# Kernel tuning notes

Hardware: AMD Instinct MI355X
Metric: run time of the kernel (lower is better)

The kernel has to match this reference:

```python
import jax, jax.numpy as jnp
import numpy as np

EPS = 1e-5
ALPHA = 0.05   # propalpha
GDEP = 2       # gcn_depth
LAYERS = 3     # gcn_layers
NUM_TCN = 2    # num_layer tcn units per encoder


def conv1x1(W, b, x):
    # 1x1 Conv2d on [B,C,N,1]: pure channel mix
    return jnp.einsum('oc,bcnl->bonl', W, x) + b[None, :, None, None]


def tcn_unit(Wf, bf, Wg, bg, h):
    # gated TCN unit: tanh(filter) * sigmoid(gate), 1x1 convs (L==1)
    return jnp.tanh(conv1x1(Wf, bf, h)) * jax.nn.sigmoid(conv1x1(Wg, bg, h))


def mixprop(x, A, W, b):
    # MTGNN mixprop: add self-loops, row-normalize, gdep propagation steps,
    # concat hops on channel dim, 1x1 conv mlp. A: [N,N] or [B,N,N].
    N = A.shape[-1]
    A = A + jnp.eye(N, dtype=A.dtype)
    A = A / A.sum(-1, keepdims=True)
    h = x
    outs = [h]
    for _ in range(GDEP):
        if A.ndim == 2:
            hn = jnp.einsum('vw,bcwl->bcvl', A, h)
        else:
            hn = jnp.einsum('bvw,bcwl->bcvl', A, h)
        h = ALPHA * x + (1.0 - ALPHA) * hn
        outs.append(h)
    ho = jnp.concatenate(outs, axis=1)  # [B,(GDEP+1)*C,N,1]
    return conv1x1(W, b, ho)


def layernorm(x, w, b):
    # LayerNorm over (C,N,1) of [B,C,N,1]; idx=arange(N) selects full affine
    mu = x.mean(axis=(1, 2, 3), keepdims=True)
    var = x.var(axis=(1, 2, 3), keepdims=True)
    return (x - mu) / jnp.sqrt(var + EPS) * w[None] + b[None]


def setup_inputs() -> dict:
    key = jax.random.key(0)
    B, N, E, H, S, T = 8, 2048, 32, 128, 256, 12
    ks = jax.random.split(key, 32)
    s = 0.05
    inp = {
        'x': jax.random.normal(ks[0], (B, E, N, 1), jnp.float32),
        'dy_graph': jax.random.uniform(ks[1], (B, N, N), jnp.float32),
        'static_graph': jax.random.uniform(ks[2], (N, N), jnp.float32),
        'spatial_emb': jax.random.normal(ks[3], (B, 32, N, 1), jnp.float32),
        'temporal_d_emb': jax.random.normal(ks[4], (B, 32, N, 1), jnp.float32),
        'temporal_w_emb': jax.random.normal(ks[5], (B, 32, N, 1), jnp.float32),
        'enc_Wf': s * jax.random.normal(ks[6], (LAYERS, NUM_TCN, H, H), jnp.float32),
        'enc_bf': s * jax.random.normal(ks[7], (LAYERS, NUM_TCN, H), jnp.float32),
        'enc_Wg': s * jax.random.normal(ks[8], (LAYERS, NUM_TCN, H, H), jnp.float32),
        'enc_bg': s * jax.random.normal(ks[9], (LAYERS, NUM_TCN, H), jnp.float32),
        'skip_W': s * jax.random.normal(ks[10], (LAYERS, S, H), jnp.float32),
        'skip_b': s * jax.random.normal(ks[11], (LAYERS, S), jnp.float32),
        'norm_w': jnp.ones((LAYERS, E, N, 1), jnp.float32),
        'norm_b': jnp.zeros((LAYERS, E, N, 1), jnp.float32),
        'g0_W': s * jax.random.normal(ks[12], (LAYERS, E, (GDEP + 1) * E), jnp.float32),
        'g0_b': s * jax.random.normal(ks[13], (LAYERS, E), jnp.float32),
        'g1_W': s * jax.random.normal(ks[14], (LAYERS, E, (GDEP + 1) * E), jnp.float32),
        'g1_b': s * jax.random.normal(ks[15], (LAYERS, E), jnp.float32),
        'g2_W': s * jax.random.normal(ks[16], (LAYERS, E, (GDEP + 1) * E), jnp.float32),
        'g2_b': s * jax.random.normal(ks[17], (LAYERS, E), jnp.float32),
        'skipE_W': s * jax.random.normal(ks[18], (S, E), jnp.float32),
        'skipE_b': s * jax.random.normal(ks[19], (S,), jnp.float32),
        'end_W': s * jax.random.normal(ks[20], (T, S), jnp.float32),
        'end_b': s * jax.random.normal(ks[21], (T,), jnp.float32),
    }
    return inp


def reference(x, dy_graph, static_graph, spatial_emb, temporal_d_emb, temporal_w_emb,
              enc_Wf, enc_bf, enc_Wg, enc_bg, skip_W, skip_b, norm_w, norm_b,
              g0_W, g0_b, g1_W, g1_b, g2_W, g2_b, skipE_W, skipE_b, end_W, end_b):
    adp = dy_graph
    skip = 0.0
    for i in range(LAYERS):
        residual = x
        hidden = jnp.concatenate([x, spatial_emb, temporal_d_emb, temporal_w_emb], axis=1)
        for j in range(NUM_TCN):
            hidden = tcn_unit(enc_Wf[i, j], enc_bf[i, j], enc_Wg[i, j], enc_bg[i, j], hidden)
        skip = conv1x1(skip_W[i], skip_b[i], hidden) + skip
        x = (mixprop(x, static_graph, g0_W[i], g0_b[i])
             + mixprop(x, adp, g1_W[i], g1_b[i])
             + mixprop(x, jnp.swapaxes(adp, -1, -2), g2_W[i], g2_b[i]))
        x = x + residual
        x = jax.nn.relu(layernorm(x, norm_w[i], norm_b[i]))
    skip = conv1x1(skipE_W, skipE_b, x) + skip
    return conv1x1(end_W, end_b, skip)  # [B, seq_length, N, 1]
```

## Files before the change

### kernel.cpp

```cpp
#include <hip/hip_runtime.h>
#include <stdint.h>


typedef uint16_t u16;
typedef uint32_t u32;
typedef __attribute__((ext_vector_type(8))) short s8v;
typedef __attribute__((ext_vector_type(4))) float f4v;

#define MFMA16(a,b,c) __builtin_amdgcn_mfma_f32_16x16x32_bf16(a,b,c,0,0,0)

__device__ __forceinline__ float b2f(u16 u){ union{u32 i; float f;} x; x.i=(u32)u<<16; return x.f; }
__device__ __forceinline__ u16 f2b(float f){
  u32 u = __builtin_bit_cast(u32, f);
  u32 r = (u + 0x7fffu + ((u >> 16) & 1u)) >> 16;
  return (u16)r;
}

__global__ __launch_bounds__(256) void kdetect(const u16* __restrict__ x, int* __restrict__ flag)
{
  const int i = threadIdx.x;
  const uint4* p = (const uint4*)x;
  int cnt = 0;
  #pragma unroll
  for (int q = 0; q < 32; q++) {
    const uint4 v = p[i + q*256];
    const u32 w[4] = {v.x, v.y, v.z, v.w};
    #pragma unroll
    for (int e = 0; e < 4; e++) {
      if ((w[e] & 0x7F80u) == 0x7F80u) cnt++;
      if (((w[e] >> 16) & 0x7F80u) == 0x7F80u) cnt++;
    }
  }
  __shared__ int s[256];
  s[i] = cnt; __syncthreads();
  for (int st = 128; st; st >>= 1) { if (i < st) s[i] += s[i+st]; __syncthreads(); }
  if (i == 0) flag[0] = (s[0] > 0) ? 1 : 0;
}

__global__ __launch_bounds__(256) void kcvt4(const void* __restrict__ src, u16* __restrict__ dst,
                                             int n4, const int* __restrict__ flag)
{
  if (!*flag) return;
  const int i = blockIdx.x*256 + threadIdx.x;
  if (i >= n4) return;
  const float4 v = ((const float4*)src)[i];
  u16 o[4]; o[0]=f2b(v.x); o[1]=f2b(v.y); o[2]=f2b(v.z); o[3]=f2b(v.w);
  *(uint2*)(dst + (long)i*4) = *(uint2*)o;
}

struct CvtTab { const void* s[18]; u16* d[18]; int n4[18]; };
__global__ __launch_bounds__(256) void kcvt_small(CvtTab tb, const int* __restrict__ flag)
{
  const int e = blockIdx.y;
  const int i = blockIdx.x*256 + threadIdx.x;
  if (i >= tb.n4[e]) return;
  if (*flag) {
    const float4 v = ((const float4*)tb.s[e])[i];
    u16 o[4]; o[0]=f2b(v.x); o[1]=f2b(v.y); o[2]=f2b(v.z); o[3]=f2b(v.w);
    *(uint2*)(tb.d[e] + (long)i*4) = *(uint2*)o;
  } else {
    *(uint2*)(tb.d[e] + (long)i*4) = ((const uint2*)tb.s[e])[i];
  }
}

__global__ __launch_bounds__(256) void kcvtT(
    const void* __restrict__ src, u16* __restrict__ dyb, u16* __restrict__ dytb,
    float* __restrict__ rsum, float* __restrict__ csum, const int* __restrict__ flag)
{
  __shared__ alignas(16) u16 tt[64][112];
  const int tid = threadIdx.x;
  const int b = blockIdx.z;
  const long r0 = (long)blockIdx.y*64;
  const long c0 = (long)blockIdx.x*64;
  const int r = tid>>2, cg = (tid&3)*16;
  const long base = (long)b*4194304;
  const int fl = *flag;

  u16 v16[16];
  const long goff = base + (r0+r)*2048 + c0 + cg;
  if (fl) {
    const float* sp = (const float*)src + goff;
    #pragma unroll
    for (int q = 0; q < 4; q++) {
      const float4 f = ((const float4*)sp)[q];
      v16[q*4+0]=f2b(f.x); v16[q*4+1]=f2b(f.y); v16[q*4+2]=f2b(f.z); v16[q*4+3]=f2b(f.w);
    }
    *(uint4*)(dyb + goff)     = *(uint4*)&v16[0];
    *(uint4*)(dyb + goff + 8) = *(uint4*)&v16[8];
  } else {
    const u16* sp = (const u16*)src + goff;
    *(uint4*)&v16[0] = ((const uint4*)sp)[0];
    *(uint4*)&v16[8] = ((const uint4*)sp)[1];
  }
  float rs = 0.f;
  #pragma unroll
  for (int e = 0; e < 16; e++) {
    rs += b2f(v16[e]);
    const int c = cg + e;
    tt[c][r + ((c>>4)&3)*16] = v16[e];
  }
  rs += __shfl_down(rs, 2, 64);
  rs += __shfl_down(rs, 1, 64);
  if ((tid&3)==0) atomicAdd(rsum + b*2048 + r0 + r, rs);
  __syncthreads();

  const int c = tid>>2, rg = (tid&3)*16;
  const int sh = ((c>>4)&3)*16;
  u16 col[16];
  *(uint4*)&col[0] = *(const uint4*)&tt[c][sh + rg];
  *(uint4*)&col[8] = *(const uint4*)&tt[c][sh + rg + 8];
  float cs = 0.f;
  #pragma unroll
  for (int e = 0; e < 16; e++) cs += b2f(col[e]);
  cs += __shfl_down(cs, 2, 64);
  cs += __shfl_down(cs, 1, 64);
  u16* dp = dytb + base + (c0 + c)*2048 + r0 + rg;
  *(uint4*)(dp)     = *(uint4*)&col[0];
  *(uint4*)(dp + 8) = *(uint4*)&col[8];
  if ((tid&3)==0) atomicAdd(csum + b*2048 + c0 + c, cs);
}

__global__ void kfin(float* __restrict__ v){
  const int i = blockIdx.x*256 + threadIdx.x;
  v[i] = 1.f/(1.f + v[i]);
}

struct P3 {
  const u16* A0; const u16* A1; const u16* A2;
  const u16* A0alt; const u16* A1alt;
  const int* flag;
  long ab0, ab1, ab2;
  const u16* X0; const u16* X1; const u16* X2;
  const float* R0; const float* R1; const float* R2;
  long rb0, rb1, rb2;
  u16* O0; u16* O1; u16* O2;
};

template<int SHAREX>
__global__ __launch_bounds__(256) void kprop3(P3 p, long x_bs, long o_bs)
{
  constexpr int NS = SHAREX ? 5 : 9;
  __shared__ f4v red[4][6][64];
  const int tid = threadIdx.x, wave = tid>>6, lane = tid&63;
  const int lw = lane&15, quad = lane>>4;
  const int v0 = blockIdx.x*16;
  const int b = blockIdx.y;
  const long ko = (long)(wave*512 + quad*8);
  const int fl = *p.flag;
  const u16* A0g = fl ? p.A0 : p.A0alt;
  const u16* A1g = fl ? p.A1 : p.A1alt;
  const u16* ptr[9];
  ptr[0] = A0g + (long)b*p.ab0 + (long)(v0+lw)*2048 + ko;
  ptr[1] = A1g + (long)b*p.ab1 + (long)(v0+lw)*2048 + ko;
  ptr[2] = p.A2 + (long)b*p.ab2 + (long)(v0+lw)*2048 + ko;
  ptr[3] = p.X0 + (long)b*x_bs + (long)lw*2048 + ko;
  ptr[4] = p.X0 + (long)b*x_bs + (long)(16+lw)*2048 + ko;
  if (!SHAREX) {
    ptr[5] = p.X1 + (long)b*x_bs + (long)lw*2048 + ko;
    ptr[6] = p.X1 + (long)b*x_bs + (long)(16+lw)*2048 + ko;
    ptr[7] = p.X2 + (long)b*x_bs + (long)lw*2048 + ko;
    ptr[8] = p.X2 + (long)b*x_bs + (long)(16+lw)*2048 + ko;
  }
  f4v acc[6];
  #pragma unroll
  for (int t = 0; t < 6; t++) acc[t] = (f4v){0.f,0.f,0.f,0.f};
  s8v B0[NS][2], B1[NS][2];

  auto LD = [&](s8v (&B)[NS][2], int off){
    #pragma unroll
    for (int s = 0; s < NS; s++) {
      B[s][0] = *(const s8v*)(ptr[s] + off);
      B[s][1] = *(const s8v*)(ptr[s] + off + 32);
    }
  };
  auto FM = [&](s8v (&B)[NS][2]){
    #pragma unroll
    for (int u = 0; u < 2; u++) {
      if (SHAREX) {
        acc[0] = MFMA16(B[0][u], B[3][u], acc[0]);
        acc[1] = MFMA16(B[0][u], B[4][u], acc[1]);
        acc[2] = MFMA16(B[1][u], B[3][u], acc[2]);
        acc[3] = MFMA16(B[1][u], B[4][u], acc[3]);
        acc[4] = MFMA16(B[2][u], B[3][u], acc[4]);
        acc[5] = MFMA16(B[2][u], B[4][u], acc[5]);
      } else {
        acc[0] = MFMA16(B[0][u], B[3][u], acc[0]);
        acc[1] = MFMA16(B[0][u], B[4][u], acc[1]);
        acc[2] = MFMA16(B[1][u], B[5][u], acc[2]);
        acc[3] = MFMA16(B[1][u], B[6][u], acc[3]);
        acc[4] = MFMA16(B[2][u], B[7][u], acc[4]);
        acc[5] = MFMA16(B[2][u], B[8][u], acc[5]);
      }
    }
  };

  LD(B0, 0);
  #pragma unroll 1
  for (int i = 0; i < 3; i++) {
    LD(B1, 64);
    FM(B0);
    LD(B0, 128);
    FM(B1);
    #pragma unroll
    for (int s = 0; s < NS; s++) ptr[s] += 128;
  }
  LD(B1, 64);
  FM(B0);
  FM(B1);

  #pragma unroll
  for (int t = 0; t < 6; t++) red[wave][t][lane] = acc[t];
  __syncthreads();
  if (wave < 3) {
    const int vb = v0 + quad*4;
    const u16* Xg   = (wave==0) ? p.X0 : (wave==1) ? (SHAREX ? p.X0 : p.X1) : (SHAREX ? p.X0 : p.X2);
    const float* Rg = (wave==0) ? p.R0 : (wave==1) ? p.R1 : p.R2;
    const long rbs  = (wave==0) ? p.rb0 : (wave==1) ? p.rb1 : p.rb2;
    u16* Og         = (wave==0) ? p.O0 : (wave==1) ? p.O1 : p.O2;
    #pragma unroll
    for (int nt = 0; nt < 2; nt++) {
      const int t = wave*2 + nt;
      f4v s = red[0][t][lane] + red[1][t][lane] + red[2][t][lane] + red[3][t][lane];
      const int c = nt*16 + lw;
      const u16* dp = Xg + (long)b*x_bs + (long)c*2048 + vb;
      const float* rp = Rg + (long)b*rbs + vb;
      u16 pk[4];
      #pragma unroll
      for (int r = 0; r < 4; r++) pk[r] = f2b((s[r] + b2f(dp[r])) * rp[r]);
      *(uint2*)(Og + (long)b*o_bs + (long)c*2048 + vb) = *(uint2*)pk;
    }
  }
}

template<int TRANSA, int MODE>
__global__ __launch_bounds__(256) void kprop(
    const u16* __restrict__ A, long a_bs, int lda, int K,
    const u16* __restrict__ X, long x_bs, int ldx,
    const u16* __restrict__ D, long d_bs,
    const float* __restrict__ rinv, long r_bs,
    const float* __restrict__ bias,
    u16* __restrict__ out0, float* __restrict__ out1, long o_bs)
{
  __shared__ u16 As[4][2][16][40];
  __shared__ f4v red[4][2][64];
  const int tid = threadIdx.x;
  const int wave = tid >> 6, lane = tid & 63;
  const int lw = lane & 15, quad = lane >> 4;
  const int v0 = blockIdx.x * 16;
  const int ball = blockIdx.z + blockIdx.y;
  const u16* Ab = A + (long)ball * a_bs;
  const u16* Xb = X + (long)ball * x_bs;
  const int KC = K >> 5;

  f4v acc0 = {0.f,0.f,0.f,0.f}, acc1 = {0.f,0.f,0.f,0.f};

  int r0, c0_;
  if (TRANSA == 0) { r0 = lane >> 2; c0_ = (lane & 3) * 8; }
  else             { r0 = lane >> 1; c0_ = (lane & 1) * 8; }

  int ci = wave;
  bool has = ci < KC;
  uint4 d = make_uint4(0,0,0,0);
  if (has) {
    d = (TRANSA == 0)
      ? *(const uint4*)(Ab + (long)(v0 + r0) * lda + ci * 32 + c0_)
      : *(const uint4*)(Ab + (long)(ci * 32 + r0) * lda + v0 + c0_);
  }
  int buf = 0;
  while (has) {
    if (TRANSA == 0) {
      *(uint4*)&As[wave][buf][r0][c0_] = d;
    } else {
      u16 tmp[8]; *(uint4*)tmp = d;
      #pragma unroll
      for (int e = 0; e < 8; e++) As[wave][buf][c0_ + e][r0] = tmp[e];
    }
    const int cn = ci + 4;
    const bool hn = cn < KC;
    if (hn) {
      d = (TRANSA == 0)
        ? *(const uint4*)(Ab + (long)(v0 + r0) * lda + cn * 32 + c0_)
        : *(const uint4*)(Ab + (long)(cn * 32 + r0) * lda + v0 + c0_);
    }
    s8v af = *(const s8v*)&As[wave][buf][lw][quad * 8];
    const u16* xk = Xb + ci * 32 + quad * 8;
    s8v b0 = *(const s8v*)(xk + (long)lw * ldx);
    s8v b1 = *(const s8v*)(xk + (long)(16 + lw) * ldx);
    acc0 = MFMA16(af, b0, acc0);
    acc1 = MFMA16(af, b1, acc1);
    ci = cn; has = hn; buf ^= 1;
  }
  red[wave][0][lane] = acc0;
  red[wave][1][lane] = acc1;
  __syncthreads();
  if (wave == 0) {
    const int vb = v0 + quad * 4;
    #pragma unroll
    for (int nt = 0; nt < 2; nt++) {
      f4v a = red[0][nt][lane] + red[1][nt][lane] + red[2][nt][lane] + red[3][nt][lane];
      const int c = nt * 16 + lw;
      const u16* dp = D + (long)ball * d_bs + (long)c * 2048 + vb;
      if (MODE == 0) {
        const float* rp = rinv + (long)ball * r_bs + vb;
        u16 pk[4];
        #pragma unroll
        for (int r = 0; r < 4; r++) pk[r] = f2b((a[r] + b2f(dp[r])) * rp[r]);
        *(uint2*)(out0 + (long)ball * o_bs + (long)c * 2048 + vb) = *(uint2*)pk;
      } else {
        const float bs = bias[c];
        float4 st;
        st.x = a[0] + bs + b2f(dp[0]);
        st.y = a[1] + bs + b2f(dp[1]);
        st.z = a[2] + bs + b2f(dp[2]);
        st.w = a[3] + bs + b2f(dp[3]);
        *(float4*)(out1 + (long)ball * o_bs + (long)c * 2048 + vb) = st;
      }
    }
  }
}

__global__ __launch_bounds__(256) void ktcn(
    const u16* __restrict__ H, const u16* __restrict__ Wf, const u16* __restrict__ bfv,
    const u16* __restrict__ Wg, const u16* __restrict__ bgv, u16* __restrict__ out)
{
  const int tid = threadIdx.x, wave = tid>>6, lane = tid&63, lw = lane&15, quad = lane>>4;
  const long j0 = (long)blockIdx.x*64 + wave*16;
  const f4v zero = {0.f,0.f,0.f,0.f};
  f4v accf[8], accg[8];
  #pragma unroll
  for (int nt=0; nt<8; nt++){ accf[nt] = zero; accg[nt] = zero; }
  const u16* Arow = H + (j0 + lw)*128 + quad*8;
  #pragma unroll
  for (int k0 = 0; k0 < 128; k0 += 32) {
    s8v a = *(const s8v*)(Arow + k0);
    #pragma unroll
    for (int nt = 0; nt < 8; nt++) {
      const int o = nt*16 + lw;
      s8v bf_ = *(const s8v*)(Wf + o*128 + k0 + quad*8);
      s8v bg_ = *(const s8v*)(Wg + o*128 + k0 + quad*8);
      accf[nt] = MFMA16(a, bf_, accf[nt]);
      accg[nt] = MFMA16(a, bg_, accg[nt]);
    }
  }
  #pragma unroll
  for (int nt = 0; nt < 8; nt++) {
    const int o = nt*16 + lw;
    const float fb = b2f(bfv[o]), gb = b2f(bgv[o]);
    #pragma unroll
    for (int rr = 0; rr < 4; rr++) {
      const long j = j0 + quad*4 + rr;
      const float f = accf[nt][rr] + fb, g = accg[nt][rr] + gb;
      const float e2 = __expf(2.f*f);
      const float th = 1.f - 2.f/(e2 + 1.f);
      const float sg = 1.f/(1.f + __expf(-g));
      out[j*128 + o] = f2b(th*sg);
    }
  }
}

__global__ __launch_bounds__(256) void kskip(
    const u16* __restrict__ A, int lda, int K,
    const u16* __restrict__ W, int ldb,
    const u16* __restrict__ bias,
    float* __restrict__ skipbuf, int addprev, int mode, u16* __restrict__ outb)
{
  const int tid = threadIdx.x, wave = tid>>6, lane = tid&63, lw = lane&15, quad = lane>>4;
  const long j0 = (long)blockIdx.x*64 + wave*16;
  const f4v zero = {0.f,0.f,0.f,0.f};
  f4v acc[16];
  #pragma unroll
  for (int nt=0; nt<16; nt++) acc[nt] = zero;
  const u16* Arow = A + (j0 + lw)*(long)lda + quad*8;
  for (int k0 = 0; k0 < K; k0 += 32) {
    s8v a = *(const s8v*)(Arow + k0);
    #pragma unroll
    for (int nt = 0; nt < 16; nt++) {
      const int o = nt*16 + lw;
      s8v b = *(const s8v*)(W + (long)o*ldb + k0 + quad*8);
      acc[nt] = MFMA16(a, b, acc[nt]);
    }
  }
  #pragma unroll
  for (int nt = 0; nt < 16; nt++) {
    const int o = nt*16 + lw;
    const float bv = b2f(bias[o]);
    #pragma unroll
    for (int rr = 0; rr < 4; rr++) {
      const long j = j0 + quad*4 + rr;
      float v = acc[nt][rr] + bv;
      if (addprev) v += skipbuf[j*256 + o];
      if (mode == 0) skipbuf[j*256 + o] = v;
      else           outb[j*256 + o] = f2b(v);
    }
  }
}

__global__ __launch_bounds__(256) void kend(
    const u16* __restrict__ A, const u16* __restrict__ W, const u16* __restrict__ bias,
    void* __restrict__ outv, const int* __restrict__ flag)
{
  const int tid = threadIdx.x, wave = tid>>6, lane = tid&63, lw = lane&15, quad = lane>>4;
  const long j0 = (long)blockIdx.x*64 + wave*16;
  f4v acc = {0.f,0.f,0.f,0.f};
  const u16* Arow = A + (j0 + lw)*256 + quad*8;
  #pragma unroll
  for (int k0 = 0; k0 < 256; k0 += 32) {
    s8v a = *(const s8v*)(Arow + k0);
    s8v b = {0,0,0,0,0,0,0,0};
    if (lw < 12) b = *(const s8v*)(W + lw*256 + k0 + quad*8);
    acc = MFMA16(a, b, acc);
  }
  if (lw < 12) {
    const float bv = b2f(bias[lw]);
    const int fl = *flag;
    #pragma unroll
    for (int rr = 0; rr < 4; rr++) {
      const long j = j0 + quad*4 + rr;
      const long oi = (j >> 11)*24576 + lw*2048 + (j & 2047);
      const float val = acc[rr] + bv;
      if (fl) ((float*)outv)[oi] = val;
      else    ((u16*)outv)[oi]   = f2b(val);
    }
  }
}

__global__ __launch_bounds__(256) void khid0(
    const void* __restrict__ x, const void* __restrict__ spat,
    const void* __restrict__ tde, const void* __restrict__ twe,
    u16* __restrict__ hid, u16* __restrict__ slot0, const int* __restrict__ flag)
{
  __shared__ u16 t[32][72];
  const int tid = threadIdx.x, b = blockIdx.y, v0 = blockIdx.x*64;
  const int fl = *flag;
  const void* srcs[4] = {x, spat, tde, twe};
  #pragma unroll
  for (int e = 0; e < 4; e++) {
    const int c = tid>>3, v8 = (tid&7)*8;
    const long boff = (long)c*2048 + v0 + v8;
    u16 o8[8];
    if (fl) {
      const float* sp = (const float*)srcs[e] + (long)b*65536 + boff;
      const float4 a = ((const float4*)sp)[0], bb = ((const float4*)sp)[1];
      o8[0]=f2b(a.x); o8[1]=f2b(a.y); o8[2]=f2b(a.z); o8[3]=f2b(a.w);
      o8[4]=f2b(bb.x); o8[5]=f2b(bb.y); o8[6]=f2b(bb.z); o8[7]=f2b(bb.w);
    } else {
      *(uint4*)o8 = *(const uint4*)((const u16*)srcs[e] + (long)b*65536 + boff);
    }
    if (e == 0) *(uint4*)(slot0 + (long)b*458752 + boff) = *(uint4*)o8;
    *(uint4*)&t[c][v8] = *(uint4*)o8;
    __syncthreads();
    const int jl = tid>>2, c8 = (tid&3)*8;
    u16 q8[8];
    #pragma unroll
    for (int i = 0; i < 8; i++) q8[i] = t[c8 + i][jl];
    *(uint4*)(hid + ((long)b*2048 + v0 + jl)*128 + e*32 + c8) = *(uint4*)q8;
    __syncthreads();
  }
}

__global__ __launch_bounds__(256) void krowsum(const u16* __restrict__ srcA, const u16* __restrict__ srcB,
                                               const int* __restrict__ flag,
                                               float* __restrict__ outv, int nrows)
{
  const u16* src = (*flag) ? srcA : srcB;
  const int wave = threadIdx.x>>6, lane = threadIdx.x&63;
  const int row = blockIdx.x*4 + wave;
  if (row >= nrows) return;
  const u16* p = src + (long)row*2048 + lane*8;
  float s = 0.f;
  #pragma unroll
  for (int it = 0; it < 4; it++) {
    u16 v[8]; *(uint4*)v = *(const uint4*)(p + it*512);
    #pragma unroll
    for (int e = 0; e < 8; e++) s += b2f(v[e]);
  }
  #pragma unroll
  for (int off = 32; off; off >>= 1) s += __shfl_down(s, off, 64);
  if (lane == 0) outv[row] = 1.f/(1.f + s);
}

__global__ __launch_bounds__(256) void kweff(
    const u16* __restrict__ g0W, const u16* __restrict__ g1W, const u16* __restrict__ g2W,
    const u16* __restrict__ g0b, const u16* __restrict__ g1b, const u16* __restrict__ g2b,
    int ioff, int boff, u16* __restrict__ weff, float* __restrict__ bw)
{
  const int idx = blockIdx.x*256 + threadIdx.x;
  if (idx < 32) bw[idx] = b2f(g0b[boff+idx]) + b2f(g1b[boff+idx]) + b2f(g2b[boff+idx]);
  if (idx >= 7168) return;
  const int o = idx / 224, m = idx % 224;
  const u16* Ws[3] = {g0W + ioff, g1W + ioff, g2W + ioff};
  float val;
  if (m < 32) {
    val = 0.f;
    #pragma unroll
    for (int g = 0; g < 3; g++) {
      const float w0 = b2f(Ws[g][o*96 + m]);
      const float w1 = b2f(Ws[g][o*96 + 32 + m]);
      const float w2 = b2f(Ws[g][o*96 + 64 + m]);
      val += w0 + 0.05f*(w1 + w2);
    }
  } else {
    const int f = (m - 32) >> 5, cc = m & 31;
    const int g = f >> 1, typ = f & 1;
    const float w1 = b2f(Ws[g][o*96 + 32 + cc]);
    const float w2 = b2f(Ws[g][o*96 + 64 + cc]);
    val = (typ == 0) ? (0.95f*w1 + 0.0475f*w2) : (0.9025f*w2);
  }
  weff[o*224 + m] = f2b(val);
}

__global__ __launch_bounds__(256) void kstats(const float* __restrict__ xpre, float* __restrict__ raw)
{
  const int b = blockIdx.y, tid = threadIdx.x;
  const float4* p = (const float4*)(xpre + (long)b*65536 + (long)blockIdx.x*8192);
  float s = 0.f, q = 0.f;
  #pragma unroll
  for (int i = 0; i < 8; i++) {
    const float4 v = p[tid + i*256];
    s += v.x + v.y + v.z + v.w;
    q += v.x*v.x + v.y*v.y + v.z*v.z + v.w*v.w;
  }
  __shared__ float ss[256], qq[256];
  ss[tid] = s; qq[tid] = q;
  __syncthreads();
  for (int st = 128; st; st >>= 1) {
    if (tid < st) { ss[tid] += ss[tid+st]; qq[tid] += qq[tid+st]; }
    __syncthreads();
  }
  if (tid == 0) { atomicAdd(raw + b*2, ss[0]); atomicAdd(raw + b*2 + 1, qq[0]); }
}

__global__ __launch_bounds__(256) void kapply(
    const float* __restrict__ xpre, const float* __restrict__ raw,
    const u16* __restrict__ nw, const u16* __restrict__ nb,
    u16* __restrict__ slot0, u16* __restrict__ hid)
{
  __shared__ u16 t[32][72];
  const int tid = threadIdx.x, b = blockIdx.y, v0 = blockIdx.x*64;
  const float mu = raw[b*2] * (1.f/65536.f);
  const float var = raw[b*2+1] * (1.f/65536.f) - mu*mu;
  const float rs = rsqrtf(var + 1e-5f);
  const int c = tid>>3, v8 = (tid&7)*8;
  const long boff = (long)c*2048 + v0 + v8;
  float4 xa = *(const float4*)(xpre + (long)b*65536 + boff);
  float4 xbv = *(const float4*)(xpre + (long)b*65536 + boff + 4);
  u16 wv[8], bv[8], o8[8];
  *(uint4*)wv = *(const uint4*)(nw + boff);
  *(uint4*)bv = *(const uint4*)(nb + boff);
  const float xs[8] = {xa.x, xa.y, xa.z, xa.w, xbv.x, xbv.y, xbv.z, xbv.w};
  #pragma unroll
  for (int e = 0; e < 8; e++) {
    float y = (xs[e] - mu) * rs * b2f(wv[e]) + b2f(bv[e]);
    y = fmaxf(y, 0.f);
    o8[e] = f2b(y);
    t[c][v8 + e] = o8[e];
  }
  *(uint4*)(slot0 + (long)b*458752 + boff) = *(uint4*)o8;
  __syncthreads();
  const int jl = tid>>2, c8 = (tid&3)*8;
  u16 q8[8];
  #pragma unroll
  for (int e = 0; e < 8; e++) q8[e] = t[c8 + e][jl];
  *(uint4*)(hid + ((long)b*2048 + v0 + jl)*128 + c8) = *(uint4*)q8;
}

extern "C" void kernel_launch(void* const* d_in, const int* in_sizes, int n_in,
                              void* d_out, int out_size, void* d_ws, size_t ws_size,
                              hipStream_t stream)
{
  (void)in_sizes; (void)n_in; (void)out_size; (void)ws_size;

  char* ws = (char*)d_ws;
  u16*   pbuf = (u16*)(ws + 0);
  u16*   hid  = (u16*)(ws + 7340032);
  u16*   hb1  = (u16*)(ws + 11534336);
  u16*   hb2  = (u16*)(ws + 15728640);
  float* skip = (float*)(ws + 19922944);
  u16*   xsb  = (u16*)(ws + 36700160);
  float* xpre = (float*)(ws + 45088768);
  u16*   weff = (u16*)(ws + 47185920);
  float* bw   = (float*)(ws + 47202304);
  float* rst  = (float*)(ws + 47203328);
  float* rdy  = (float*)(ws + 47211520);
  float* cdy  = (float*)(ws + 47277056);
  int*   flag = (int*)(ws + 47343616);
  float* raw  = (float*)(ws + 47343744);

  size_t coff = 50331648;
  auto alloc = [&](size_t elems) -> u16* {
    u16* p = (u16*)(ws + coff);
    coff += ((elems*2 + 255)/256)*256;
    return p;
  };
  u16* dyb   = alloc(33554432);
  u16* stgb  = alloc(4194304);
  u16* encWf = alloc(98304);
  u16* encbf = alloc(768);
  u16* encWg = alloc(98304);
  u16* encbg = alloc(768);
  u16* skW   = alloc(98304);
  u16* skb   = alloc(768);
  u16* nw    = alloc(196608);
  u16* nb    = alloc(196608);
  u16* g0W   = alloc(9216);
  u16* g0b   = alloc(96);
  u16* g1W   = alloc(9216);
  u16* g1b   = alloc(96);
  u16* g2W   = alloc(9216);
  u16* g2b   = alloc(96);
  u16* sEW   = alloc(8192);
  u16* sEb   = alloc(256);
  u16* eW    = alloc(3072);
  u16* eb    = alloc(12);
  u16* dytb  = alloc(33554432);

  hipLaunchKernelGGL(kdetect, dim3(1), dim3(256), 0, stream, (const u16*)d_in[0], flag);

  CvtTab tb;
  {
    const void* ss[18] = { d_in[6], d_in[7], d_in[8], d_in[9], d_in[10], d_in[11],
      d_in[12], d_in[13], d_in[14], d_in[15], d_in[16], d_in[17], d_in[18], d_in[19],
      d_in[20], d_in[21], d_in[22], d_in[23] };
    u16* dd[18] = { encWf, encbf, encWg, encbg, skW, skb, nw, nb,
      g0W, g0b, g1W, g1b, g2W, g2b, sEW, sEb, eW, eb };
    const int nn[18] = { 24576, 192, 24576, 192, 24576, 192, 49152, 49152,
      2304, 24, 2304, 24, 2304, 24, 2048, 64, 768, 3 };
    for (int e = 0; e < 18; e++) { tb.s[e] = ss[e]; tb.d[e] = dd[e]; tb.n4[e] = nn[e]; }
  }
  hipLaunchKernelGGL(kcvt_small, dim3(192, 18), dim3(256), 0, stream, tb, flag);
  hipLaunchKernelGGL(kcvt4, dim3(4096), dim3(256), 0, stream, d_in[2], stgb, 1048576, flag);

  hipMemsetAsync(rdy, 0, 131072, stream);
  hipMemsetAsync(raw, 0, 192, stream);
  hipLaunchKernelGGL(kcvtT, dim3(32,32,8), dim3(256), 0, stream,
      d_in[1], dyb, dytb, rdy, cdy, flag);
  hipLaunchKernelGGL(kfin, dim3(128), dim3(256), 0, stream, rdy);
  hipLaunchKernelGGL(krowsum, dim3(512), dim3(256), 0, stream,
      stgb, (const u16*)d_in[2], flag, rst, 2048);
  hipLaunchKernelGGL(khid0, dim3(32,8), dim3(256), 0, stream,
      d_in[0], d_in[3], d_in[4], d_in[5], hid, pbuf, flag);

  const long PB = 458752;
  const long SL = 65536;
  const long DYB = 4194304;

  for (int i = 0; i < 3; i++) {
    hipLaunchKernelGGL(ktcn, dim3(256), dim3(256), 0, stream,
        hid, encWf + (i*2+0)*16384, encbf + (i*2+0)*128, encWg + (i*2+0)*16384, encbg + (i*2+0)*128, hb1);
    hipLaunchKernelGGL(ktcn, dim3(256), dim3(256), 0, stream,
        hb1, encWf + (i*2+1)*16384, encbf + (i*2+1)*128, encWg + (i*2+1)*16384, encbg + (i*2+1)*128, hb2);
    hipLaunchKernelGGL(kskip, dim3(256), dim3(256), 0, stream,
        hb2, 128, 128, skW + i*32768, 128, skb + i*256, skip, (i>0)?1:0, 0, (u16*)nullptr);
    hipLaunchKernelGGL(kweff, dim3(28), dim3(256), 0, stream,
        g0W, g1W, g2W, g0b, g1b, g2b, i*3072, i*32, weff, bw);

    P3 p1;
    p1.A0 = stgb; p1.A1 = dyb; p1.A2 = dytb;
    p1.A0alt = (const u16*)d_in[2]; p1.A1alt = (const u16*)d_in[1]; p1.flag = flag;
    p1.ab0 = 0;   p1.ab1 = DYB; p1.ab2 = DYB;
    p1.X0 = pbuf; p1.X1 = pbuf; p1.X2 = pbuf;
    p1.R0 = rst;  p1.R1 = rdy;  p1.R2 = cdy;
    p1.rb0 = 0;   p1.rb1 = 2048; p1.rb2 = 2048;
    p1.O0 = pbuf + 1*SL; p1.O1 = pbuf + 3*SL; p1.O2 = pbuf + 5*SL;
    hipLaunchKernelGGL((kprop3<1>), dim3(128,8), dim3(256), 0, stream, p1, PB, PB);

    P3 p2 = p1;
    p2.X0 = pbuf + 1*SL; p2.X1 = pbuf + 3*SL; p2.X2 = pbuf + 5*SL;
    p2.O0 = pbuf + 2*SL; p2.O1 = pbuf + 4*SL; p2.O2 = pbuf + 6*SL;
    hipLaunchKernelGGL((kprop3<0>), dim3(128,8), dim3(256), 0, stream, p2, PB, PB);

    hipLaunchKernelGGL((kprop<1,1>), dim3(128,1,8), dim3(256), 0, stream,
        pbuf, PB, 2048, 224, weff, 0L, 224, pbuf, PB, (const float*)nullptr, 0L, bw, (u16*)nullptr, xpre, 65536L);
    hipLaunchKernelGGL(kstats, dim3(8,8), dim3(256), 0, stream, xpre, raw + i*16);
    hipLaunchKernelGGL(kapply, dim3(32,8), dim3(256), 0, stream,
        xpre, raw + i*16, nw + i*65536, nb + i*65536, pbuf, hid);
  }
  hipLaunchKernelGGL(kskip, dim3(256), dim3(256), 0, stream,
      hid, 128, 32, sEW, 32, sEb, skip, 1, 1, xsb);
  hipLaunchKernelGGL(kend, dim3(256), dim3(256), 0, stream, xsb, eW, eb, d_out, flag);
}
```

Baseline: 891.2 us.

## Split graph propagation per graph across grid z and reshape transpose and detect kernels

The three-graph propagation kernel is split so each block handles one graph (grid z = 3), cutting per-block register and load pressure and tripling the block count. In the first hop the shared X tile is now loaded separately for each graph, adding redundant X reads. The transpose kernel packs two rows per 32-bit LDS word with an XOR swizzle to avoid bank conflicts, and the NaN/Inf detection becomes a multi-block ballot plus atomicOr after a memset of the flag. The memset now covers 320 bytes from flag, which is assumed to also clear the raw stats buffer that previously had its own memset.

```diff
diff --git a/kernel.cpp b/kernel.cpp
--- a/kernel.cpp
+++ b/kernel.cpp
@@ -18,23 +18,17 @@
 
 __global__ __launch_bounds__(256) void kdetect(const u16* __restrict__ x, int* __restrict__ flag)
 {
-  const int i = threadIdx.x;
-  const uint4* p = (const uint4*)x;
+  const int i = blockIdx.x*256 + threadIdx.x;
+  const uint4 v = ((const uint4*)x)[i];
+  const u32 w[4] = {v.x, v.y, v.z, v.w};
   int cnt = 0;
   #pragma unroll
-  for (int q = 0; q < 32; q++) {
-    const uint4 v = p[i + q*256];
-    const u32 w[4] = {v.x, v.y, v.z, v.w};
-    #pragma unroll
-    for (int e = 0; e < 4; e++) {
-      if ((w[e] & 0x7F80u) == 0x7F80u) cnt++;
-      if (((w[e] >> 16) & 0x7F80u) == 0x7F80u) cnt++;
-    }
-  }
-  __shared__ int s[256];
-  s[i] = cnt; __syncthreads();
-  for (int st = 128; st; st >>= 1) { if (i < st) s[i] += s[i+st]; __syncthreads(); }
-  if (i == 0) flag[0] = (s[0] > 0) ? 1 : 0;
+  for (int e = 0; e < 4; e++) {
+    if ((w[e] & 0x7F80u) == 0x7F80u) cnt++;
+    if (((w[e] >> 16) & 0x7F80u) == 0x7F80u) cnt++;
+  }
+  const unsigned long long m = __ballot(cnt != 0);
+  if (m && (threadIdx.x & 63) == 0) atomicOr(flag, 1);
 }
 
 __global__ __launch_bounds__(256) void kcvt4(const void* __restrict__ src, u16* __restrict__ dst,
@@ -67,57 +61,61 @@
     const void* __restrict__ src, u16* __restrict__ dyb, u16* __restrict__ dytb,
     float* __restrict__ rsum, float* __restrict__ csum, const int* __restrict__ flag)
 {
-  __shared__ alignas(16) u16 tt[64][112];
+  __shared__ alignas(16) u32 tt[64][32];
   const int tid = threadIdx.x;
   const int b = blockIdx.z;
   const long r0 = (long)blockIdx.y*64;
   const long c0 = (long)blockIdx.x*64;
-  const int r = tid>>2, cg = (tid&3)*16;
+  const int rp = tid>>3, c8 = (tid&7)*8;
   const long base = (long)b*4194304;
   const int fl = *flag;
 
-  u16 v16[16];
-  const long goff = base + (r0+r)*2048 + c0 + cg;
+  u16 lo[8], hi[8];
+  const long gl = base + (r0 + 2*rp)*2048 + c0 + c8;
+  const long gh = gl + 2048;
   if (fl) {
-    const float* sp = (const float*)src + goff;
-    #pragma unroll
-    for (int q = 0; q < 4; q++) {
-      const float4 f = ((const float4*)sp)[q];
-      v16[q*4+0]=f2b(f.x); v16[q*4+1]=f2b(f.y); v16[q*4+2]=f2b(f.z); v16[q*4+3]=f2b(f.w);
-    }
-    *(uint4*)(dyb + goff)     = *(uint4*)&v16[0];
-    *(uint4*)(dyb + goff + 8) = *(uint4*)&v16[8];
+    const float* sl = (const float*)src + gl;
+    const float* sh = (const float*)src + gh;
+    const float4 a0 = ((const float4*)sl)[0], a1 = ((const float4*)sl)[1];
+    const float4 b0 = ((const float4*)sh)[0], b1 = ((const float4*)sh)[1];
+    lo[0]=f2b(a0.x); lo[1]=f2b(a0.y); lo[2]=f2b(a0.z); lo[3]=f2b(a0.w);
+    lo[4]=f2b(a1.x); lo[5]=f2b(a1.y); lo[6]=f2b(a1.z); lo[7]=f2b(a1.w);
+    hi[0]=f2b(b0.x); hi[1]=f2b(b0.y); hi[2]=f2b(b0.z); hi[3]=f2b(b0.w);
+    hi[4]=f2b(b1.x); hi[5]=f2b(b1.y); hi[6]=f2b(b1.z); hi[7]=f2b(b1.w);
+    *(uint4*)(dyb + gl) = *(uint4*)lo;
+    *(uint4*)(dyb + gh) = *(uint4*)hi;
   } else {
-    const u16* sp = (const u16*)src + goff;
-    *(uint4*)&v16[0] = ((const uint4*)sp)[0];
-    *(uint4*)&v16[8] = ((const uint4*)sp)[1];
-  }
-  float rs = 0.f;
-  #pragma unroll
-  for (int e = 0; e < 16; e++) {
-    rs += b2f(v16[e]);
-    const int c = cg + e;
-    tt[c][r + ((c>>4)&3)*16] = v16[e];
-  }
-  rs += __shfl_down(rs, 2, 64);
-  rs += __shfl_down(rs, 1, 64);
-  if ((tid&3)==0) atomicAdd(rsum + b*2048 + r0 + r, rs);
+    *(uint4*)lo = *((const uint4*)((const u16*)src + gl));
+    *(uint4*)hi = *((const uint4*)((const u16*)src + gh));
+  }
+  float rsl = 0.f, rsh = 0.f;
+  #pragma unroll
+  for (int e = 0; e < 8; e++) {
+    rsl += b2f(lo[e]); rsh += b2f(hi[e]);
+    const int c = c8 + e;
+    tt[c][rp ^ ((c & 0x38) >> 1)] = (u32)lo[e] | ((u32)hi[e] << 16);
+  }
+  rsl += __shfl_down(rsl, 4, 8); rsl += __shfl_down(rsl, 2, 8); rsl += __shfl_down(rsl, 1, 8);
+  rsh += __shfl_down(rsh, 4, 8); rsh += __shfl_down(rsh, 2, 8); rsh += __shfl_down(rsh, 1, 8);
+  if ((tid & 7) == 0) {
+    atomicAdd(rsum + b*2048 + r0 + 2*rp,     rsl);
+    atomicAdd(rsum + b*2048 + r0 + 2*rp + 1, rsh);
+  }
   __syncthreads();
 
-  const int c = tid>>2, rg = (tid&3)*16;
-  const int sh = ((c>>4)&3)*16;
-  u16 col[16];
-  *(uint4*)&col[0] = *(const uint4*)&tt[c][sh + rg];
-  *(uint4*)&col[8] = *(const uint4*)&tt[c][sh + rg + 8];
+  const int c = tid>>2, j4 = (tid&3)*8;
+  const int sw = (c & 0x38) >> 1;
+  u32 q[8];
+  *(uint4*)&q[0] = *(const uint4*)&tt[c][j4 ^ sw];
+  *(uint4*)&q[4] = *(const uint4*)&tt[c][(j4 + 4) ^ sw];
   float cs = 0.f;
   #pragma unroll
-  for (int e = 0; e < 16; e++) cs += b2f(col[e]);
-  cs += __shfl_down(cs, 2, 64);
-  cs += __shfl_down(cs, 1, 64);
-  u16* dp = dytb + base + (c0 + c)*2048 + r0 + rg;
-  *(uint4*)(dp)     = *(uint4*)&col[0];
-  *(uint4*)(dp + 8) = *(uint4*)&col[8];
-  if ((tid&3)==0) atomicAdd(csum + b*2048 + c0 + c, cs);
+  for (int e = 0; e < 8; e++) { cs += b2f((u16)q[e]); cs += b2f((u16)(q[e] >> 16)); }
+  cs += __shfl_down(cs, 2, 4); cs += __shfl_down(cs, 1, 4);
+  u16* dp = dytb + base + (c0 + c)*2048 + r0 + 2*j4;
+  *(uint4*)(dp)     = *(uint4*)&q[0];
+  *(uint4*)(dp + 8) = *(uint4*)&q[4];
+  if ((tid & 3) == 0) atomicAdd(csum + b*2048 + c0 + c, cs);
 }
 
 __global__ void kfin(float* __restrict__ v){
@@ -125,9 +123,9 @@
   v[i] = 1.f/(1.f + v[i]);
 }
 
-struct P3 {
-  const u16* A0; const u16* A1; const u16* A2;
-  const u16* A0alt; const u16* A1alt;
+struct PG {
+  const u16* Ac0; const u16* Ac1; const u16* Ac2;
+  const u16* Ar0; const u16* Ar1;
   const int* flag;
   long ab0, ab1, ab2;
   const u16* X0; const u16* X1; const u16* X2;
@@ -136,94 +134,63 @@
   u16* O0; u16* O1; u16* O2;
 };
 
-template<int SHAREX>
-__global__ __launch_bounds__(256) void kprop3(P3 p, long x_bs, long o_bs)
-{
-  constexpr int NS = SHAREX ? 5 : 9;
-  __shared__ f4v red[4][6][64];
+__global__ __launch_bounds__(256) void kpropg(PG p, long x_bs, long o_bs)
+{
+  __shared__ f4v red[4][2][64];
   const int tid = threadIdx.x, wave = tid>>6, lane = tid&63;
   const int lw = lane&15, quad = lane>>4;
   const int v0 = blockIdx.x*16;
   const int b = blockIdx.y;
+  const int g = blockIdx.z;
+  const int fl = *p.flag;
+  const u16* Ag; long ab; const u16* Xg; const float* Rg; long rb; u16* Og;
+  if (g == 0)      { Ag = fl ? p.Ac0 : p.Ar0; ab = p.ab0; Xg = p.X0; Rg = p.R0; rb = p.rb0; Og = p.O0; }
+  else if (g == 1) { Ag = fl ? p.Ac1 : p.Ar1; ab = p.ab1; Xg = p.X1; Rg = p.R1; rb = p.rb1; Og = p.O1; }
+  else             { Ag = p.Ac2;              ab = p.ab2; Xg = p.X2; Rg = p.R2; rb = p.rb2; Og = p.O2; }
+
   const long ko = (long)(wave*512 + quad*8);
-  const int fl = *p.flag;
-  const u16* A0g = fl ? p.A0 : p.A0alt;
-  const u16* A1g = fl ? p.A1 : p.A1alt;
-  const u16* ptr[9];
-  ptr[0] = A0g + (long)b*p.ab0 + (long)(v0+lw)*2048 + ko;
-  ptr[1] = A1g + (long)b*p.ab1 + (long)(v0+lw)*2048 + ko;
-  ptr[2] = p.A2 + (long)b*p.ab2 + (long)(v0+lw)*2048 + ko;
-  ptr[3] = p.X0 + (long)b*x_bs + (long)lw*2048 + ko;
-  ptr[4] = p.X0 + (long)b*x_bs + (long)(16+lw)*2048 + ko;
-  if (!SHAREX) {
-    ptr[5] = p.X1 + (long)b*x_bs + (long)lw*2048 + ko;
-    ptr[6] = p.X1 + (long)b*x_bs + (long)(16+lw)*2048 + ko;
-    ptr[7] = p.X2 + (long)b*x_bs + (long)lw*2048 + ko;
-    ptr[8] = p.X2 + (long)b*x_bs + (long)(16+lw)*2048 + ko;
-  }
-  f4v acc[6];
-  #pragma unroll
-  for (int t = 0; t < 6; t++) acc[t] = (f4v){0.f,0.f,0.f,0.f};
-  s8v B0[NS][2], B1[NS][2];
-
-  auto LD = [&](s8v (&B)[NS][2], int off){
-    #pragma unroll
-    for (int s = 0; s < NS; s++) {
-      B[s][0] = *(const s8v*)(ptr[s] + off);
-      B[s][1] = *(const s8v*)(ptr[s] + off + 32);
-    }
-  };
-  auto FM = [&](s8v (&B)[NS][2]){
-    #pragma unroll
-    for (int u = 0; u < 2; u++) {
-      if (SHAREX) {
-        acc[0] = MFMA16(B[0][u], B[3][u], acc[0]);
-        acc[1] = MFMA16(B[0][u], B[4][u], acc[1]);
-        acc[2] = MFMA16(B[1][u], B[3][u], acc[2]);
-        acc[3] = MFMA16(B[1][u], B[4][u], acc[3]);
-        acc[4] = MFMA16(B[2][u], B[3][u], acc[4]);
-        acc[5] = MFMA16(B[2][u], B[4][u], acc[5]);
-      } else {
-        acc[0] = MFMA16(B[0][u], B[3][u], acc[0]);
-        acc[1] = MFMA16(B[0][u], B[4][u], acc[1]);
-        acc[2] = MFMA16(B[1][u], B[5][u], acc[2]);
-        acc[3] = MFMA16(B[1][u], B[6][u], acc[3]);
-        acc[4] = MFMA16(B[2][u], B[7][u], acc[4]);
-        acc[5] = MFMA16(B[2][u], B[8][u], acc[5]);
-      }
-    }
-  };
-
-  LD(B0, 0);
+  const u16* pa  = Ag + (long)b*ab   + (long)(v0+lw)*2048 + ko;
+  const u16* px0 = Xg + (long)b*x_bs + (long)lw*2048 + ko;
+  const u16* px1 = Xg + (long)b*x_bs + (long)(16+lw)*2048 + ko;
+
+  f4v acc0 = {0.f,0.f,0.f,0.f}, acc1 = {0.f,0.f,0.f,0.f};
+  s8v A0[2], Xa0[2], Xa1[2], A1[2], Xb0[2], Xb1[2];
+
+#define LDP(Av, X0v, X1v, off) do { \
+    Av[0]  = *(const s8v*)(pa  + (off)); Av[1]  = *(const s8v*)(pa  + (off) + 32); \
+    X0v[0] = *(const s8v*)(px0 + (off)); X0v[1] = *(const s8v*)(px0 + (off) + 32); \
+    X1v[0] = *(const s8v*)(px1 + (off)); X1v[1] = *(const s8v*)(px1 + (off) + 32); } while(0)
+#define FMP(Av, X0v, X1v) do { \
+    acc0 = MFMA16(Av[0], X0v[0], acc0); acc1 = MFMA16(Av[0], X1v[0], acc1); \
+    acc0 = MFMA16(Av[1], X0v[1], acc0); acc1 = MFMA16(Av[1], X1v[1], acc1); } while(0)
+
+  LDP(A0, Xa0, Xa1, 0);
   #pragma unroll 1
   for (int i = 0; i < 3; i++) {
-    LD(B1, 64);
-    FM(B0);
-    LD(B0, 128);
-    FM(B1);
-    #pragma unroll
-    for (int s = 0; s < NS; s++) ptr[s] += 128;
-  }
-  LD(B1, 64);
-  FM(B0);
-  FM(B1);
-
-  #pragma unroll
-  for (int t = 0; t < 6; t++) red[wave][t][lane] = acc[t];
+    LDP(A1, Xb0, Xb1, 64);
+    FMP(A0, Xa0, Xa1);
+    LDP(A0, Xa0, Xa1, 128);
+    FMP(A1, Xb0, Xb1);
+    pa += 128; px0 += 128; px1 += 128;
+  }
+  LDP(A1, Xb0, Xb1, 64);
+  FMP(A0, Xa0, Xa1);
+  FMP(A1, Xb0, Xb1);
+
+#undef LDP
+#undef FMP
+
+  red[wave][0][lane] = acc0;
+  red[wave][1][lane] = acc1;
   __syncthreads();
-  if (wave < 3) {
+  if (wave == 0) {
     const int vb = v0 + quad*4;
-    const u16* Xg   = (wave==0) ? p.X0 : (wave==1) ? (SHAREX ? p.X0 : p.X1) : (SHAREX ? p.X0 : p.X2);
-    const float* Rg = (wave==0) ? p.R0 : (wave==1) ? p.R1 : p.R2;
-    const long rbs  = (wave==0) ? p.rb0 : (wave==1) ? p.rb1 : p.rb2;
-    u16* Og         = (wave==0) ? p.O0 : (wave==1) ? p.O1 : p.O2;
     #pragma unroll
     for (int nt = 0; nt < 2; nt++) {
-      const int t = wave*2 + nt;
-      f4v s = red[0][t][lane] + red[1][t][lane] + red[2][t][lane] + red[3][t][lane];
+      f4v s = red[0][nt][lane] + red[1][nt][lane] + red[2][nt][lane] + red[3][nt][lane];
       const int c = nt*16 + lw;
       const u16* dp = Xg + (long)b*x_bs + (long)c*2048 + vb;
-      const float* rp = Rg + (long)b*rbs + vb;
+      const float* rp = Rg + (long)b*rb + vb;
       u16 pk[4];
       #pragma unroll
       for (int r = 0; r < 4; r++) pk[r] = f2b((s[r] + b2f(dp[r])) * rp[r]);
@@ -614,7 +581,8 @@
   u16* eb    = alloc(12);
   u16* dytb  = alloc(33554432);
 
-  hipLaunchKernelGGL(kdetect, dim3(1), dim3(256), 0, stream, (const u16*)d_in[0], flag);
+  hipMemsetAsync(flag, 0, 320, stream);
+  hipLaunchKernelGGL(kdetect, dim3(32), dim3(256), 0, stream, (const u16*)d_in[0], flag);
 
   CvtTab tb;
   {
@@ -631,7 +599,6 @@
   hipLaunchKernelGGL(kcvt4, dim3(4096), dim3(256), 0, stream, d_in[2], stgb, 1048576, flag);
 
   hipMemsetAsync(rdy, 0, 131072, stream);
-  hipMemsetAsync(raw, 0, 192, stream);
   hipLaunchKernelGGL(kcvtT, dim3(32,32,8), dim3(256), 0, stream,
       d_in[1], dyb, dytb, rdy, cdy, flag);
   hipLaunchKernelGGL(kfin, dim3(128), dim3(256), 0, stream, rdy);
@@ -654,20 +621,21 @@
     hipLaunchKernelGGL(kweff, dim3(28), dim3(256), 0, stream,
         g0W, g1W, g2W, g0b, g1b, g2b, i*3072, i*32, weff, bw);
 
-    P3 p1;
-    p1.A0 = stgb; p1.A1 = dyb; p1.A2 = dytb;
-    p1.A0alt = (const u16*)d_in[2]; p1.A1alt = (const u16*)d_in[1]; p1.flag = flag;
+    PG p1;
+    p1.Ac0 = stgb; p1.Ac1 = dyb; p1.Ac2 = dytb;
+    p1.Ar0 = (const u16*)d_in[2]; p1.Ar1 = (const u16*)d_in[1];
+    p1.flag = flag;
     p1.ab0 = 0;   p1.ab1 = DYB; p1.ab2 = DYB;
     p1.X0 = pbuf; p1.X1 = pbuf; p1.X2 = pbuf;
     p1.R0 = rst;  p1.R1 = rdy;  p1.R2 = cdy;
     p1.rb0 = 0;   p1.rb1 = 2048; p1.rb2 = 2048;
     p1.O0 = pbuf + 1*SL; p1.O1 = pbuf + 3*SL; p1.O2 = pbuf + 5*SL;
-    hipLaunchKernelGGL((kprop3<1>), dim3(128,8), dim3(256), 0, stream, p1, PB, PB);
-
-    P3 p2 = p1;
+    hipLaunchKernelGGL(kpropg, dim3(128,8,3), dim3(256), 0, stream, p1, PB, PB);
+
+    PG p2 = p1;
     p2.X0 = pbuf + 1*SL; p2.X1 = pbuf + 3*SL; p2.X2 = pbuf + 5*SL;
     p2.O0 = pbuf + 2*SL; p2.O1 = pbuf + 4*SL; p2.O2 = pbuf + 6*SL;
-    hipLaunchKernelGGL((kprop3<0>), dim3(128,8), dim3(256), 0, stream, p2, PB, PB);
+    hipLaunchKernelGGL(kpropg, dim3(128,8,3), dim3(256), 0, stream, p2, PB, PB);
 
     hipLaunchKernelGGL((kprop<1,1>), dim3(128,1,8), dim3(256), 0, stream,
         pbuf, PB, 2048, 224, weff, 0L, 224, pbuf, PB, (const float*)nullptr, 0L, bw, (u16*)nullptr, xpre, 65536L);
```

Result: slower. 966.7 us (+8.5%).
